# Optimization experiments

Hardware: AMD Instinct MI355X
Metric: run time of the kernel (lower is better)

## Reference

```python
import jax, jax.numpy as jnp
import numpy as np

B, H, W, N = 8, 384, 384, 96
STEPSZ = 0.1; ALPHA = 0.01; BETA = 0.01; STD = 1.0
NSTEPS = 50; NSTEPS_W = 10; DMAX = 15.0; EXTGRADFAC = 10.0

def make_gauss_edge_fltr(std):
    # Gaussian-derivative edge filters, one per spatial dim: [2,1,k,k]
    r = int(np.ceil(3 * std)); t = np.arange(-r, r + 1, dtype=np.float32)
    g = np.exp(-t * t / (2 * std * std)); g /= g.sum()
    dg = -t / (std * std) * np.exp(-t * t / (2 * std * std)); dg /= np.abs(dg).sum()
    fy = np.outer(dg, g)   # d/drow
    fx = np.outer(g, dg)   # d/dcol
    return np.stack([fy, fx])[:, None].astype(np.float32)

def setup_inputs() -> dict:
    key = jax.random.key(0)
    k1, k2 = jax.random.split(key, 2)
    pred_dmap = jax.random.normal(k1, (B, 1, H, W), jnp.float32)
    nodes = jax.random.uniform(k2, (B, N, 2), jnp.float32)
    nodes = nodes * jnp.array([H - 1.0, W - 1.0], jnp.float32)
    nodes = jnp.sort(nodes, axis=1)  # roughly monotone chain -> path-like snake
    widths = jnp.ones((B, N), jnp.float32) * 3.0
    fltr = jnp.asarray(make_gauss_edge_fltr(STD))
    return {"pred_dmap": pred_dmap, "nodes": nodes, "widths": widths, "fltr": fltr}

def grad_im(x, fltr):
    # x: [B,1,H,W], fltr: [2,1,k,k] -> [B,2,H,W]
    return jax.lax.conv_general_dilated(x, fltr, (1, 1), 'SAME',
                                        dimension_numbers=('NCHW', 'OIHW', 'NCHW'))

def interp(img, pts):
    # bilinear sample: img [C,H,W], pts [N,2] (row,col) -> [N,C]
    C, Hh, Ww = img.shape
    y = jnp.clip(pts[:, 0], 0.0, Hh - 1.0); x = jnp.clip(pts[:, 1], 0.0, Ww - 1.0)
    y0 = jnp.floor(y).astype(jnp.int32); x0 = jnp.floor(x).astype(jnp.int32)
    y1 = jnp.minimum(y0 + 1, Hh - 1); x1 = jnp.minimum(x0 + 1, Ww - 1)
    wy = y - y0; wx = x - x0
    v00 = img[:, y0, x0]; v01 = img[:, y0, x1]
    v10 = img[:, y1, x0]; v11 = img[:, y1, x1]
    v = v00 * (1 - wy) * (1 - wx) + v01 * (1 - wy) * wx + v10 * wy * (1 - wx) + v11 * wy * wx
    return v.T

def d2_open(x):
    # second difference with replicated endpoints (open snake)
    xp = jnp.concatenate([x[:1], x, x[-1:]], 0)
    return xp[:-2] - 2 * xp[1:-1] + xp[2:]

def snake_one(nodes, widths, g, gw):
    # explicit active-contour iterations on node positions
    def pstep(x, _):
        fext = interp(g, x)                       # [N,2] external force
        d2 = d2_open(x); d4 = d2_open(d2)
        return x + STEPSZ * (ALPHA * d2 - BETA * d4 + fext), None
    x, _ = jax.lax.scan(pstep, nodes, None, length=NSTEPS)
    # unit normals from central-difference tangents
    t = jnp.concatenate([x[1:2] - x[0:1], 0.5 * (x[2:] - x[:-2]), x[-1:] - x[-2:-1]], 0)
    n = jnp.stack([-t[:, 1], t[:, 0]], 1)
    n = n / (jnp.linalg.norm(n, axis=1, keepdims=True) + 1e-6)
    def wstep(w, _):
        gp = interp(gw, x + w[:, None] * n); gm = interp(gw, x - w[:, None] * n)
        f = 0.5 * (jnp.sum(gp * n, 1) - jnp.sum(gm * n, 1))
        return jnp.maximum(w + STEPSZ * f, 0.5), None
    w, _ = jax.lax.scan(wstep, widths, None, length=NSTEPS_W)
    return x, w

def render(x, w):
    # distance-to-ribbon map, clipped at DMAX; only [HW,S] intermediates
    ys, xs = jnp.meshgrid(jnp.arange(H, dtype=jnp.float32),
                          jnp.arange(W, dtype=jnp.float32), indexing='ij')
    P = jnp.stack([ys.ravel(), xs.ravel()], 1)          # [HW,2]
    a = x[:-1]; ab = x[1:] - a                          # [S,2]
    denom = jnp.sum(ab * ab, 1) + 1e-8                  # [S]
    dotpa = P @ ab.T - jnp.sum(a * ab, 1)               # [HW,S] = (P-a).ab
    t = jnp.clip(dotpa / denom, 0.0, 1.0)
    pa2 = jnp.sum(P * P, 1)[:, None] - 2 * (P @ a.T) + jnp.sum(a * a, 1)  # |P-a|^2
    d = jnp.sqrt(jnp.maximum(pa2 - 2 * t * dotpa + t * t * denom, 0.0))
    ws = 0.5 * (w[:-1] + w[1:])                         # per-segment width
    dmap = jnp.min(jnp.maximum(d - ws, 0.0), axis=1)
    return jnp.minimum(dmap, DMAX).reshape(H, W)

def reference(pred_dmap, nodes, widths, fltr):
    gimg = grad_im(pred_dmap, fltr) * EXTGRADFAC          # [B,2,H,W]
    gimgW = grad_im(jnp.abs(pred_dmap), fltr) * EXTGRADFAC
    def per_sample(nd, wd, g, gw):
        x, w = snake_one(nd, wd, g, gw)
        return render(x, w)
    dm = jax.vmap(per_sample)(nodes, widths, gimg, gimgW)[:, None]  # [B,1,H,W]
    dm = jax.lax.stop_gradient(dm)   # snake_dm.detach() in the original
    return jnp.mean((pred_dmap - dm) ** 2)
```

## Files before the change

kernel.cpp:

```cpp
#include <hip/hip_runtime.h>
#include <math.h>

#define BB   8
#define HH   384
#define WW   384
#define NN   96
#define HWSZ (HH * WW)
#define NSEG (NN - 1)
#define SEGF 12
#define SEGPAD 1152
#define DMAXV 15.0f
#define ROWS_PER_BLK 12
#define NCHUNK (HH / ROWS_PER_BLK)
#define CROWS 12
#define CBANDS (HH / CROWS)
#define MAGICU 0x9E3779B9u

typedef unsigned long long u64;
typedef unsigned int u32;

__device__ inline void st_pair(float* p, float lo, float hi)
{
    u64 v = ((u64)__float_as_uint(hi) << 32) | (u64)__float_as_uint(lo);
    __hip_atomic_store((u64*)p, v, __ATOMIC_RELAXED, __HIP_MEMORY_SCOPE_AGENT);
}

__device__ inline float ld_f32_coh(const float* p)
{
    u32 v = __hip_atomic_load((u32*)p, __ATOMIC_RELAXED, __HIP_MEMORY_SCOPE_AGENT);
    return __uint_as_float(v);
}

#define WAIT_ALL() asm volatile("s_waitcnt vmcnt(0) lgkmcnt(0)" ::: "memory")

__device__ inline void load_taps(const float* __restrict__ fltr,
                                 float* __restrict__ sg, float* __restrict__ sdg)
{
    int tid = threadIdx.x;
    if (tid < 7) {
        float s = 0.f;
#pragma unroll
        for (int i = 0; i < 7; ++i) s += fabsf(fltr[i * 7 + tid]);
        sg[tid] = s;
    } else if (tid < 14) {
        int r = tid - 7;
        float s = 0.f;
#pragma unroll
        for (int j = 0; j < 7; ++j) s += fltr[r * 7 + j];
        sdg[r] = s;
    }
    __syncthreads();
}

__global__ __launch_bounds__(384) void conv_fused(
    const float* __restrict__ pred, const float* __restrict__ fltr,
    float2* __restrict__ g2, float2* __restrict__ gw2)
{
    __shared__ float sg[7], sdg[7];
    load_taps(fltr, sg, sdg);

    int blk = blockIdx.x;
    int b = blk & 7;
    int band = blk >> 3;
    int y0 = band * CROWS;
    int x = threadIdx.x;
    const float* pb = pred + (size_t)b * HWSZ;
    bool xin = (x >= 3) && (x < WW - 3);

    float hg[7], hd[7], hga[7], hda[7];

#pragma unroll
    for (int q = 0; q < CROWS + 6; ++q) {
        float vg = 0.f, vd = 0.f, vga = 0.f, vda = 0.f;
        int r = y0 + q - 3;
        if (r >= 0 && r < HH) {
            const float* row = pb + r * WW;
            if (xin) {
#pragma unroll
                for (int k = 0; k < 7; ++k) {
                    float v  = row[x + k - 3];
                    float av = fabsf(v);
                    vg  = fmaf(v,  sg[k],  vg);
                    vd  = fmaf(v,  sdg[k], vd);
                    vga = fmaf(av, sg[k],  vga);
                    vda = fmaf(av, sdg[k], vda);
                }
            } else {
#pragma unroll
                for (int k = 0; k < 7; ++k) {
                    int ix = x + k - 3;
                    float v  = (ix >= 0 && ix < WW) ? row[ix] : 0.f;
                    float av = fabsf(v);
                    vg  = fmaf(v,  sg[k],  vg);
                    vd  = fmaf(v,  sdg[k], vd);
                    vga = fmaf(av, sg[k],  vga);
                    vda = fmaf(av, sdg[k], vda);
                }
            }
        }
        hg[q % 7] = vg; hd[q % 7] = vd; hga[q % 7] = vga; hda[q % 7] = vda;

        if (q >= 6) {
            int y = y0 + q - 6;
            float o0 = 0.f, o1 = 0.f, o2 = 0.f, o3 = 0.f;
#pragma unroll
            for (int j = 0; j < 7; ++j) {
                int s = (q - 6 + j) % 7;
                o0 = fmaf(hg[s],  sdg[j], o0);
                o1 = fmaf(hd[s],  sg[j],  o1);
                o2 = fmaf(hga[s], sdg[j], o2);
                o3 = fmaf(hda[s], sg[j],  o3);
            }
            size_t gi = (size_t)b * HWSZ + (size_t)y * WW + x;
            g2[gi]  = make_float2(o0 * 10.f, o1 * 10.f);
            gw2[gi] = make_float2(o2 * 10.f, o3 * 10.f);
        }
    }
}

__device__ inline float2 bilin2i(const float2* __restrict__ img, float py, float px)
{
    float y = fminf(fmaxf(py, 0.0f), (float)(HH - 1));
    float x = fminf(fmaxf(px, 0.0f), (float)(WW - 1));
    int y0 = (int)floorf(y);
    int x0 = (int)floorf(x);
    int y1 = min(y0 + 1, HH - 1);
    bool xedge = (x0 + 1 > WW - 1);
    float wy = y - (float)y0;
    float wx = x - (float)x0;
    float4 r0 = *(const float4*)(img + y0 * WW + x0);
    float4 r1 = *(const float4*)(img + y1 * WW + x0);
    float2 v00 = make_float2(r0.x, r0.y);
    float2 v01 = xedge ? v00 : make_float2(r0.z, r0.w);
    float2 v10 = make_float2(r1.x, r1.y);
    float2 v11 = xedge ? v10 : make_float2(r1.z, r1.w);
    float w00 = (1.f - wy) * (1.f - wx);
    float w01 = (1.f - wy) * wx;
    float w10 = wy * (1.f - wx);
    float w11 = wy * wx;
    return make_float2(v00.x * w00 + v01.x * w01 + v10.x * w10 + v11.x * w11,
                       v00.y * w00 + v01.y * w01 + v10.y * w10 + v11.y * w11);
}

__device__ inline void write_seg_wt(float* __restrict__ r,
                                    float py, float px, float qy, float qx, float wseg)
{
    float aby = qy - py, abx = qx - px;
    float denom = aby * aby + abx * abx + 1e-8f;
    float aab = py * aby + px * abx;
    float aa  = py * py + px * px;
    float reach = DMAXV + wseg;
    st_pair(r + 0,  py,  px);
    st_pair(r + 2,  aby, abx);
    st_pair(r + 4,  aab, denom);
    st_pair(r + 6,  1.0f / denom, aa);
    st_pair(r + 8,  wseg, fminf(py, qy) - reach);
    st_pair(r + 10, fmaxf(py, qy) + reach, 0.f);
}

__global__ __launch_bounds__(384) void snake_render(
    const float* __restrict__ pred, const float* __restrict__ nodes,
    const float* __restrict__ widths,
    const float* __restrict__ g2f, const float* __restrict__ gw2f,
    float* __restrict__ segs, u64* __restrict__ pflag,
    u32* __restrict__ segflag, float* __restrict__ out)
{
    __shared__ float ss[NSEG * SEGF];
    __shared__ int slo, shi;
    __shared__ float swsum[6];

    int blk = blockIdx.x;
    int b   = blk & 7;
    int band = blk >> 3;
    int t = threadIdx.x;

    int y0r = band * ROWS_PER_BLK;
    const float* pb = pred + (size_t)b * HWSZ + (size_t)y0r * WW + t;
    float pv[ROWS_PER_BLK];
#pragma unroll
    for (int ry = 0; ry < ROWS_PER_BLK; ++ry) pv[ry] = pb[ry * WW];

    if (t == 0) { slo = NSEG; shi = -1; }

    if (blk < 8 && t < 64) {
        const float2* gb  = (const float2*)g2f  + (size_t)b * HWSZ;
        const float2* gwb = (const float2*)gw2f + (size_t)b * HWSZ;
        const int HALF = NN / 2;
        bool act = (t < HALF);
        bool t0 = (t == 0), tl = (t == HALF - 1);

        float ay = 0.f, ax = 0.f, by = 0.f, bx = 0.f;
        if (act) {
            float4 n4 = *(const float4*)(nodes + (size_t)(b * NN + 2 * t) * 2);
            ay = n4.x; ax = n4.y; by = n4.z; bx = n4.w;
        }

        for (int s = 0; s < 50; ++s) {
            float2 fa = bilin2i(gb, ay, ax);
            float2 fb = bilin2i(gb, by, bx);

            float aLy = __shfl_up(ay, 1, 64),  aLx = __shfl_up(ax, 1, 64);
            float bLy = __shfl_up(by, 1, 64),  bLx = __shfl_up(bx, 1, 64);
            float aRy = __shfl_down(ay, 1, 64), aRx = __shfl_down(ax, 1, 64);
            float bRy = __shfl_down(by, 1, 64), bRx = __shfl_down(bx, 1, 64);
            bLy = t0 ? ay : bLy;  bLx = t0 ? ax : bLx;
            aRy = tl ? by : aRy;  aRx = tl ? bx : aRx;

            float d2m_y = aLy - 2.f * bLy + ay;
            float d2a_y = bLy - 2.f * ay + by;
            float d2b_y = ay  - 2.f * by + aRy;
            float d2p_y = by  - 2.f * aRy + bRy;
            d2m_y = t0 ? d2a_y : d2m_y;
            d2p_y = tl ? d2b_y : d2p_y;
            float d4a_y = d2m_y - 2.f * d2a_y + d2b_y;
            float d4b_y = d2a_y - 2.f * d2b_y + d2p_y;

            float d2m_x = aLx - 2.f * bLx + ax;
            float d2a_x = bLx - 2.f * ax + bx;
            float d2b_x = ax  - 2.f * bx + aRx;
            float d2p_x = bx  - 2.f * aRx + bRx;
            d2m_x = t0 ? d2a_x : d2m_x;
            d2p_x = tl ? d2b_x : d2p_x;
            float d4a_x = d2m_x - 2.f * d2a_x + d2b_x;
            float d4b_x = d2a_x - 2.f * d2b_x + d2p_x;

            ay += 0.1f * (0.01f * d2a_y - 0.01f * d4a_y + fa.x);
            ax += 0.1f * (0.01f * d2a_x - 0.01f * d4a_x + fa.y);
            by += 0.1f * (0.01f * d2b_y - 0.01f * d4b_y + fb.x);
            bx += 0.1f * (0.01f * d2b_x - 0.01f * d4b_x + fb.y);
        }

        {
            float bLy = __shfl_up(by, 1, 64), bLx = __shfl_up(bx, 1, 64);
            float aRy = __shfl_down(ay, 1, 64), aRx = __shfl_down(ax, 1, 64);
            float tay = 0.5f * (by - bLy), tax = 0.5f * (bx - bLx);
            if (t0) { tay = by - ay; tax = bx - ax; }
            float tby = 0.5f * (aRy - ay), tbx = 0.5f * (aRx - ax);
            if (tl) { tby = by - ay; tbx = bx - ax; }

            float na0 = -tax, na1 = tay;
            float nrm = sqrtf(na0 * na0 + na1 * na1) + 1e-6f;
            float nay = na0 / nrm, nax = na1 / nrm;
            float nb0 = -tbx, nb1 = tby;
            nrm = sqrtf(nb0 * nb0 + nb1 * nb1) + 1e-6f;
            float nby = nb0 / nrm, nbx = nb1 / nrm;

            float wa = 0.f, wb = 0.f;
            if (act) { wa = widths[b * NN + 2 * t]; wb = widths[b * NN + 2 * t + 1]; }
            for (int s = 0; s < 10; ++s) {
                float2 pa = bilin2i(gwb, ay + wa * nay, ax + wa * nax);
                float2 ma = bilin2i(gwb, ay - wa * nay, ax - wa * nax);
                float2 pb2 = bilin2i(gwb, by + wb * nby, bx + wb * nbx);
                float2 mb = bilin2i(gwb, by - wb * nby, bx - wb * nbx);
                float fa = 0.5f * ((pa.x * nay + pa.y * nax) - (ma.x * nay + ma.y * nax));
                float fb = 0.5f * ((pb2.x * nby + pb2.y * nbx) - (mb.x * nby + mb.y * nbx));
                wa = fmaxf(wa + 0.1f * fa, 0.5f);
                wb = fmaxf(wb + 0.1f * fb, 0.5f);
            }

            float aRy2 = __shfl_down(ay, 1, 64), aRx2 = __shfl_down(ax, 1, 64);
            float waR  = __shfl_down(wa, 1, 64);
            float* segb = segs + (size_t)b * SEGPAD;
            if (act) {
                write_seg_wt(segb + (size_t)(2 * t) * SEGF, ay, ax, by, bx,
                             0.5f * (wa + wb));
                if (t < HALF - 1)
                    write_seg_wt(segb + (size_t)(2 * t + 1) * SEGF, by, bx, aRy2, aRx2,
                                 0.5f * (wb + waR));
            }
        }
        WAIT_ALL();
        if (t == 0)
            __hip_atomic_store(&segflag[b], MAGICU,
                               __ATOMIC_RELAXED, __HIP_MEMORY_SCOPE_AGENT);
    } else if (blk >= 8 && t == 0) {
        while (__hip_atomic_load(&segflag[b],
                                 __ATOMIC_RELAXED, __HIP_MEMORY_SCOPE_AGENT) != MAGICU)
            __builtin_amdgcn_s_sleep(8);
        asm volatile("" ::: "memory");
    }

    __syncthreads();

    {
        int y0 = y0r;
        const float* sb = segs + (size_t)b * SEGPAD;
        for (int j = t; j < NSEG * SEGF; j += 384)
            ss[j] = ld_f32_coh(sb + j);
        __syncthreads();

        float cy0 = (float)y0, cy1 = (float)(y0 + ROWS_PER_BLK - 1);
        if (t < NSEG) {
            float ylo = ss[t * SEGF + 9];
            float yhi = ss[t * SEGF + 10];
            if (yhi >= cy0 && ylo <= cy1) {
                atomicMin(&slo, t);
                atomicMax(&shi, t);
            }
        }
        __syncthreads();
        int lo = slo, hi = shi;

        float px = (float)t;
        float px2 = px * px;
        float minv[ROWS_PER_BLK];
#pragma unroll
        for (int r = 0; r < ROWS_PER_BLK; ++r) minv[r] = DMAXV;

        for (int si = lo; si <= hi; ++si) {
            const float* r = ss + si * SEGF;
            float ax = r[1], abx = r[3], ws = r[8];
            float bxe = ax + abx;
            float reach = DMAXV + ws + 0.01f;
            if (px < fminf(ax, bxe) - reach || px > fmaxf(ax, bxe) + reach) continue;

            float ay = r[0], aby = r[2];
            float aab = r[4], denom = r[5], invd = r[6], aa = r[7];
            float dotpa_b = fmaf(px, abx, -aab);
            float pa2_b   = fmaf(px, -2.0f * ax, px2 + aa);
#pragma unroll
            for (int ry = 0; ry < ROWS_PER_BLK; ++ry) {
                float py = (float)(y0 + ry);
                float dotpa = fmaf(py, aby, dotpa_b);
                float tt = fminf(fmaxf(dotpa * invd, 0.0f), 1.0f);
                float pa2 = fmaf(py, fmaf(py, 1.0f, -2.0f * ay), pa2_b);
                float d2 = fmaf(tt, fmaf(tt, denom, -2.0f * dotpa), pa2);
                float d = sqrtf(fmaxf(d2, 0.0f));
                float v = fmaxf(d - ws, 0.0f);
                minv[ry] = fminf(minv[ry], v);
            }
        }

        float sq = 0.f;
#pragma unroll
        for (int ry = 0; ry < ROWS_PER_BLK; ++ry) {
            float diff = pv[ry] - minv[ry];
            sq = fmaf(diff, diff, sq);
        }

#pragma unroll
        for (int off = 32; off > 0; off >>= 1) sq += __shfl_down(sq, off, 64);
        if ((t & 63) == 0) swsum[t >> 6] = sq;
        __syncthreads();
        if (t == 0) {
            float tot = swsum[0] + swsum[1] + swsum[2] + swsum[3] + swsum[4] + swsum[5];
            u64 pvv = ((u64)MAGICU << 32) | (u64)__float_as_uint(tot);
            __hip_atomic_store(&pflag[blk], pvv,
                               __ATOMIC_RELAXED, __HIP_MEMORY_SCOPE_AGENT);
        }
    }

    if (blk == 8) {
        __syncthreads();
        float v = 0.f;
        if (t < 256) {
            u64 pvv = __hip_atomic_load(&pflag[t], __ATOMIC_RELAXED,
                                        __HIP_MEMORY_SCOPE_AGENT);
            while ((u32)(pvv >> 32) != MAGICU) {
                __builtin_amdgcn_s_sleep(4);
                pvv = __hip_atomic_load(&pflag[t], __ATOMIC_RELAXED,
                                        __HIP_MEMORY_SCOPE_AGENT);
            }
            v = __uint_as_float((u32)pvv);
        }
#pragma unroll
        for (int off = 32; off > 0; off >>= 1) v += __shfl_down(v, off, 64);
        if ((t & 63) == 0) swsum[t >> 6] = v;
        __syncthreads();
        if (t == 0) {
            float tot = swsum[0] + swsum[1] + swsum[2] + swsum[3] + swsum[4] + swsum[5];
            out[0] = tot * (1.0f / (float)(BB * HWSZ));
        }
    }
}

extern "C" void kernel_launch(void* const* d_in, const int* in_sizes, int n_in,
                              void* d_out, int out_size, void* d_ws, size_t ws_size,
                              hipStream_t stream)
{
    const float* pred   = (const float*)d_in[0];
    const float* nodes  = (const float*)d_in[1];
    const float* widths = (const float*)d_in[2];
    const float* fltr   = (const float*)d_in[3];
    float* out = (float*)d_out;

    float* ws   = (float*)d_ws;
    float* g2   = ws;
    float* gw2  = g2 + (size_t)2 * BB * HWSZ;
    float* segs = gw2 + (size_t)2 * BB * HWSZ;
    float* tail = segs + (size_t)BB * SEGPAD + 256;
    u64* pflag = (u64*)tail;
    u32* segflag = (u32*)(pflag + 256);

    conv_fused<<<BB * CBANDS, 384, 0, stream>>>(pred, fltr,
                                                (float2*)g2, (float2*)gw2);
    snake_render<<<BB * NCHUNK, 384, 0, stream>>>(pred, nodes, widths, g2, gw2,
                                                  segs, pflag, segflag, out);
}
```

Before: 127.1 us.

## Spread snake iterations over two wavefronts with one node per thread via LDS

```diff
diff --git a/kernel.cpp b/kernel.cpp
--- a/kernel.cpp
+++ b/kernel.cpp
@@ -166,6 +166,8 @@
     u32* __restrict__ segflag, float* __restrict__ out)
 {
     __shared__ float ss[NSEG * SEGF];
+    __shared__ float2 posb[2][NN];
+    __shared__ float  wbuf[NN];
     __shared__ int slo, shi;
     __shared__ float swsum[6];
 
@@ -182,102 +184,115 @@
 
     if (t == 0) { slo = NSEG; shi = -1; }
 
-    if (blk < 8 && t < 64) {
+    if (blk < 8) {
         const float2* gb  = (const float2*)g2f  + (size_t)b * HWSZ;
         const float2* gwb = (const float2*)gw2f + (size_t)b * HWSZ;
-        const int HALF = NN / 2;
-        bool act = (t < HALF);
-        bool t0 = (t == 0), tl = (t == HALF - 1);
-
-        float ay = 0.f, ax = 0.f, by = 0.f, bx = 0.f;
+        int wv = t >> 6, ln = t & 63;
+        int n  = wv * 48 + ln;
+        bool act = (wv < 2) && (ln < 48);
+        bool n0f = (n == 0), nlf = (n == NN - 1);
+
+        float py = 0.f, px = 0.f;
         if (act) {
-            float4 n4 = *(const float4*)(nodes + (size_t)(b * NN + 2 * t) * 2);
-            ay = n4.x; ax = n4.y; by = n4.z; bx = n4.w;
-        }
+            float2 p0 = *(const float2*)(nodes + (size_t)(b * NN + n) * 2);
+            py = p0.x; px = p0.y;
+            posb[0][n] = p0;
+        }
+        __syncthreads();
 
         for (int s = 0; s < 50; ++s) {
-            float2 fa = bilin2i(gb, ay, ax);
-            float2 fb = bilin2i(gb, by, bx);
-
-            float aLy = __shfl_up(ay, 1, 64),  aLx = __shfl_up(ax, 1, 64);
-            float bLy = __shfl_up(by, 1, 64),  bLx = __shfl_up(bx, 1, 64);
-            float aRy = __shfl_down(ay, 1, 64), aRx = __shfl_down(ax, 1, 64);
-            float bRy = __shfl_down(by, 1, 64), bRx = __shfl_down(bx, 1, 64);
-            bLy = t0 ? ay : bLy;  bLx = t0 ? ax : bLx;
-            aRy = tl ? by : aRy;  aRx = tl ? bx : aRx;
-
-            float d2m_y = aLy - 2.f * bLy + ay;
-            float d2a_y = bLy - 2.f * ay + by;
-            float d2b_y = ay  - 2.f * by + aRy;
-            float d2p_y = by  - 2.f * aRy + bRy;
-            d2m_y = t0 ? d2a_y : d2m_y;
-            d2p_y = tl ? d2b_y : d2p_y;
-            float d4a_y = d2m_y - 2.f * d2a_y + d2b_y;
-            float d4b_y = d2a_y - 2.f * d2b_y + d2p_y;
-
-            float d2m_x = aLx - 2.f * bLx + ax;
-            float d2a_x = bLx - 2.f * ax + bx;
-            float d2b_x = ax  - 2.f * bx + aRx;
-            float d2p_x = bx  - 2.f * aRx + bRx;
-            d2m_x = t0 ? d2a_x : d2m_x;
-            d2p_x = tl ? d2b_x : d2p_x;
-            float d4a_x = d2m_x - 2.f * d2a_x + d2b_x;
-            float d4b_x = d2a_x - 2.f * d2b_x + d2p_x;
-
-            ay += 0.1f * (0.01f * d2a_y - 0.01f * d4a_y + fa.x);
-            ax += 0.1f * (0.01f * d2a_x - 0.01f * d4a_x + fa.y);
-            by += 0.1f * (0.01f * d2b_y - 0.01f * d4b_y + fb.x);
-            bx += 0.1f * (0.01f * d2b_x - 0.01f * d4b_x + fb.y);
-        }
-
-        {
-            float bLy = __shfl_up(by, 1, 64), bLx = __shfl_up(bx, 1, 64);
-            float aRy = __shfl_down(ay, 1, 64), aRx = __shfl_down(ax, 1, 64);
-            float tay = 0.5f * (by - bLy), tax = 0.5f * (bx - bLx);
-            if (t0) { tay = by - ay; tax = bx - ax; }
-            float tby = 0.5f * (aRy - ay), tbx = 0.5f * (aRx - ax);
-            if (tl) { tby = by - ay; tbx = bx - ax; }
-
-            float na0 = -tax, na1 = tay;
-            float nrm = sqrtf(na0 * na0 + na1 * na1) + 1e-6f;
-            float nay = na0 / nrm, nax = na1 / nrm;
-            float nb0 = -tbx, nb1 = tby;
-            nrm = sqrtf(nb0 * nb0 + nb1 * nb1) + 1e-6f;
-            float nby = nb0 / nrm, nbx = nb1 / nrm;
-
-            float wa = 0.f, wb = 0.f;
-            if (act) { wa = widths[b * NN + 2 * t]; wb = widths[b * NN + 2 * t + 1]; }
+            const float2* pcur = posb[s & 1];
+            float2* pnxt = posb[(s & 1) ^ 1];
+            if (act) {
+                float yc = fminf(fmaxf(py, 0.0f), (float)(HH - 1));
+                float xc = fminf(fmaxf(px, 0.0f), (float)(WW - 1));
+                int y0i = (int)floorf(yc);
+                int x0i = (int)floorf(xc);
+                int y1i = min(y0i + 1, HH - 1);
+                bool xedge = (x0i + 1 > WW - 1);
+                float wy = yc - (float)y0i;
+                float wx = xc - (float)x0i;
+                float4 r0 = *(const float4*)(gb + y0i * WW + x0i);
+                float4 r1 = *(const float4*)(gb + y1i * WW + x0i);
+
+                float2 xm1 = pcur[max(n - 1, 0)];
+                float2 xp1 = pcur[min(n + 1, NN - 1)];
+                float2 xm2 = pcur[max(n - 2, 0)];
+                float2 xp2 = pcur[min(n + 2, NN - 1)];
+
+                float d2m_y = xm2.x - 2.f * xm1.x + py;
+                float d2c_y = xm1.x - 2.f * py + xp1.x;
+                float d2p_y = py - 2.f * xp1.x + xp2.x;
+                float d2m_x = xm2.y - 2.f * xm1.y + px;
+                float d2c_x = xm1.y - 2.f * px + xp1.y;
+                float d2p_x = px - 2.f * xp1.y + xp2.y;
+                d2m_y = n0f ? d2c_y : d2m_y;
+                d2m_x = n0f ? d2c_x : d2m_x;
+                d2p_y = nlf ? d2c_y : d2p_y;
+                d2p_x = nlf ? d2c_x : d2p_x;
+                float d4_y = d2m_y - 2.f * d2c_y + d2p_y;
+                float d4_x = d2m_x - 2.f * d2c_x + d2p_x;
+
+                float2 v00 = make_float2(r0.x, r0.y);
+                float2 v01 = xedge ? v00 : make_float2(r0.z, r0.w);
+                float2 v10 = make_float2(r1.x, r1.y);
+                float2 v11 = xedge ? v10 : make_float2(r1.z, r1.w);
+                float w00 = (1.f - wy) * (1.f - wx);
+                float w01 = (1.f - wy) * wx;
+                float w10 = wy * (1.f - wx);
+                float w11 = wy * wx;
+                float fy = v00.x * w00 + v01.x * w01 + v10.x * w10 + v11.x * w11;
+                float fx = v00.y * w00 + v01.y * w01 + v10.y * w10 + v11.y * w11;
+
+                py += 0.1f * (0.01f * d2c_y - 0.01f * d4_y + fy);
+                px += 0.1f * (0.01f * d2c_x - 0.01f * d4_x + fx);
+                pnxt[n] = make_float2(py, px);
+            }
+            __syncthreads();
+        }
+
+        float ny_ = 0.f, nx_ = 0.f, wn = 0.f;
+        if (act) {
+            float2 xm1 = posb[0][max(n - 1, 0)];
+            float2 xp1 = posb[0][min(n + 1, NN - 1)];
+            float ty, tx;
+            if (n0f)      { ty = xp1.x - py;  tx = xp1.y - px; }
+            else if (nlf) { ty = py - xm1.x;  tx = px - xm1.y; }
+            else          { ty = 0.5f * (xp1.x - xm1.x); tx = 0.5f * (xp1.y - xm1.y); }
+
+            float nn0 = -tx, nn1 = ty;
+            float nrm = sqrtf(nn0 * nn0 + nn1 * nn1) + 1e-6f;
+            ny_ = nn0 / nrm; nx_ = nn1 / nrm;
+
+            wn = widths[b * NN + n];
             for (int s = 0; s < 10; ++s) {
-                float2 pa = bilin2i(gwb, ay + wa * nay, ax + wa * nax);
-                float2 ma = bilin2i(gwb, ay - wa * nay, ax - wa * nax);
-                float2 pb2 = bilin2i(gwb, by + wb * nby, bx + wb * nbx);
-                float2 mb = bilin2i(gwb, by - wb * nby, bx - wb * nbx);
-                float fa = 0.5f * ((pa.x * nay + pa.y * nax) - (ma.x * nay + ma.y * nax));
-                float fb = 0.5f * ((pb2.x * nby + pb2.y * nbx) - (mb.x * nby + mb.y * nbx));
-                wa = fmaxf(wa + 0.1f * fa, 0.5f);
-                wb = fmaxf(wb + 0.1f * fb, 0.5f);
-            }
-
-            float aRy2 = __shfl_down(ay, 1, 64), aRx2 = __shfl_down(ax, 1, 64);
-            float waR  = __shfl_down(wa, 1, 64);
-            float* segb = segs + (size_t)b * SEGPAD;
-            if (act) {
-                write_seg_wt(segb + (size_t)(2 * t) * SEGF, ay, ax, by, bx,
-                             0.5f * (wa + wb));
-                if (t < HALF - 1)
-                    write_seg_wt(segb + (size_t)(2 * t + 1) * SEGF, by, bx, aRy2, aRx2,
-                                 0.5f * (wb + waR));
-            }
+                float2 gp = bilin2i(gwb, py + wn * ny_, px + wn * nx_);
+                float2 gm = bilin2i(gwb, py - wn * ny_, px - wn * nx_);
+                float fw = 0.5f * ((gp.x * ny_ + gp.y * nx_) - (gm.x * ny_ + gm.y * nx_));
+                wn = fmaxf(wn + 0.1f * fw, 0.5f);
+            }
+            wbuf[n] = wn;
+        }
+        __syncthreads();
+
+        if (act && n < NSEG) {
+            float2 q = posb[0][n + 1];
+            float wq = wbuf[n + 1];
+            write_seg_wt(segs + (size_t)b * SEGPAD + (size_t)n * SEGF,
+                         py, px, q.x, q.y, 0.5f * (wn + wq));
         }
         WAIT_ALL();
+        __syncthreads();
         if (t == 0)
             __hip_atomic_store(&segflag[b], MAGICU,
                                __ATOMIC_RELAXED, __HIP_MEMORY_SCOPE_AGENT);
-    } else if (blk >= 8 && t == 0) {
-        while (__hip_atomic_load(&segflag[b],
-                                 __ATOMIC_RELAXED, __HIP_MEMORY_SCOPE_AGENT) != MAGICU)
-            __builtin_amdgcn_s_sleep(8);
-        asm volatile("" ::: "memory");
+    } else {
+        if (t == 0) {
+            while (__hip_atomic_load(&segflag[b],
+                                     __ATOMIC_RELAXED, __HIP_MEMORY_SCOPE_AGENT) != MAGICU)
+                __builtin_amdgcn_s_sleep(8);
+            asm volatile("" ::: "memory");
+        }
     }
 
     __syncthreads();
```

Result: faster. 121.3 us (-4.6%).
